# Kernel optimization log

Measured on AMD Instinct MI355X. Metric: run time of the kernel, lower is better.

## Reference

```python
import jax, jax.numpy as jnp
import numpy as np

KERNEL_SIZE = 4  # kernel_size=4, dim=1, degree-1 open B-splines (SplineConv defaults)


def spline_conv(x, edge_index, edge_attr, W, root, bias):
    """SplineConv with dim=1, kernel_size=4, degree=1, open splines, aggr='mean'.

    x: [N, F_in]; edge_index: [2, E] (row 0 = source, row 1 = target);
    edge_attr: [E, 1] pseudo-coords in [0,1]; W: [K, F_in, F_out];
    root: [F_in, F_out]; bias: [F_out].
    """
    N = x.shape[0]
    src, dst = edge_index[0], edge_index[1]
    u = edge_attr[:, 0]                          # [E]
    v = u * (KERNEL_SIZE - 1)                    # open spline: scale by K-1
    vf = jnp.floor(v)
    frac = v - vf                                # [E], degree-1 basis fraction
    k0 = jnp.clip(vf.astype(jnp.int32), 0, KERNEL_SIZE - 1)
    k1 = jnp.minimum(k0 + 1, KERNEL_SIZE - 1)
    # Project node features through all K kernel weights once: [N, K, F_out]
    xw = jnp.einsum('nf,kfo->nko', x, W)
    # Per-edge message: basis-weighted mix of the two active kernel projections
    m = (1.0 - frac)[:, None] * xw[src, k0] + frac[:, None] * xw[src, k1]  # [E, F_out]
    # Mean aggregation at target nodes
    agg = jax.ops.segment_sum(m, dst, num_segments=N)               # [N, F_out]
    deg = jax.ops.segment_sum(jnp.ones_like(u), dst, num_segments=N)
    agg = agg / jnp.maximum(deg, 1.0)[:, None]
    return agg + x @ root + bias


def setup_inputs() -> dict:
    key = jax.random.key(0)
    ks = jax.random.split(key, 9)
    N, E, F_IN, HID, C = 50000, 1600000, 48, 32, 10
    x = jax.random.normal(ks[0], (N, F_IN), dtype=jnp.float32)
    edge_index = jax.random.randint(ks[1], (2, E), 0, N, dtype=jnp.int64)
    edge_attr = jax.random.uniform(ks[2], (E, 1), dtype=jnp.float32)
    s = 0.1
    W1 = jax.random.normal(ks[3], (KERNEL_SIZE, F_IN, HID), dtype=jnp.float32) * s
    root1 = jax.random.normal(ks[4], (F_IN, HID), dtype=jnp.float32) * s
    bias1 = jax.random.normal(ks[5], (HID,), dtype=jnp.float32) * s
    W2 = jax.random.normal(ks[6], (KERNEL_SIZE, HID, C), dtype=jnp.float32) * s
    root2 = jax.random.normal(ks[7], (HID, C), dtype=jnp.float32) * s
    bias2 = jax.random.normal(ks[8], (C,), dtype=jnp.float32) * s
    return {"x": x, "edge_index": edge_index, "edge_attr": edge_attr,
            "W1": W1, "root1": root1, "bias1": bias1,
            "W2": W2, "root2": root2, "bias2": bias2}


def reference(x, edge_index, edge_attr, W1, root1, bias1, W2, root2, bias2):
    # dropout is identity in eval mode (training=self.training)
    h = spline_conv(x, edge_index, edge_attr, W1, root1, bias1)
    h = jax.nn.elu(h)
    h = spline_conv(h, edge_index, edge_attr, W2, root2, bias2)
    return jax.nn.log_softmax(h, axis=1)
```

## Files before the change

kernel.cpp:

```cpp
#include <hip/hip_runtime.h>
#include <math.h>


#define F_IN   48
#define HID    32
#define NCLS   10
#define KS     4
#define BKT_SH 8
#define TILE   4096

__device__ inline unsigned short f2bf(float f) {
    unsigned x = __float_as_uint(f);
    unsigned r = x + 0x7FFFu + ((x >> 16) & 1u);
    return (unsigned short)(r >> 16);
}
__device__ inline float bf2f(unsigned short u) {
    return __uint_as_float(((unsigned)u) << 16);
}


__global__ void bucket_hist_kernel(const int* __restrict__ ei, int* __restrict__ bcnt,
                                   int E, int NB) {
    __shared__ int lcnt[256];
    int t = threadIdx.x;
    lcnt[t] = 0;
    __syncthreads();
    int e0 = blockIdx.x * TILE;
    int n = min(TILE, E - e0);
    for (int r = 0; r < TILE / 256; ++r) {
        int i = r * 256 + t;
        if (i < n) atomicAdd(&lcnt[ei[E + e0 + i] >> BKT_SH], 1);
    }
    __syncthreads();
    if (t < NB && lcnt[t] > 0) atomicAdd(&bcnt[t], lcnt[t]);
}

__global__ void mini_scan_kernel(const int* __restrict__ bcnt, int* __restrict__ bbase,
                                 int* __restrict__ gcur, int NB) {
    __shared__ int a[256], c[256];
    int t = threadIdx.x;
    int v = (t < NB) ? bcnt[t] : 0;
    a[t] = v; c[t] = v;
    __syncthreads();
    for (int o = 1; o < 256; o <<= 1) {
        int w = (t >= o) ? a[t - o] : 0;
        __syncthreads();
        a[t] += w;
        __syncthreads();
    }
    int ex = a[t] - c[t];
    if (t < NB) { bbase[t] = ex; gcur[t] = ex; }
    if (t == 0) bbase[NB] = a[255];
}

__global__ void bucket_scatter_kernel(const int* __restrict__ ei, const float* __restrict__ ea,
                                      int* __restrict__ gcur, uint2* __restrict__ tpd,
                                      int E, int NB) {
    __shared__ unsigned spl[TILE];
    __shared__ unsigned short sdst[TILE];
    __shared__ unsigned short inv[TILE];
    __shared__ int lcnt[256], loff[256], lrank[256], gb[256];
    int t = threadIdx.x;
    lcnt[t] = 0; lrank[t] = 0;
    __syncthreads();
    int e0 = blockIdx.x * TILE;
    int n = min(TILE, E - e0);
    for (int r = 0; r < TILE / 256; ++r) {
        int i = r * 256 + t;
        if (i < n) {
            int e = e0 + i;
            int src = ei[e];
            int dst = ei[E + e];
            float u = ea[e];
            float v = u * (float)(KS - 1);
            float vf = floorf(v);
            int k0 = min(max((int)vf, 0), KS - 1);
            unsigned qf = (unsigned)((v - vf) * 16383.f + 0.5f);
            spl[i] = (unsigned)src | ((unsigned)k0 << 16) | (qf << 18);
            sdst[i] = (unsigned short)dst;
            atomicAdd(&lcnt[dst >> BKT_SH], 1);
        }
    }
    __syncthreads();
    loff[t] = lcnt[t];
    __syncthreads();
    for (int o = 1; o < 256; o <<= 1) {
        int w = (t >= o) ? loff[t - o] : 0;
        __syncthreads();
        loff[t] += w;
        __syncthreads();
    }
    int ex = loff[t] - lcnt[t];
    __syncthreads();
    loff[t] = ex;
    if (t < NB) gb[t] = atomicAdd(&gcur[t], lcnt[t]);
    __syncthreads();
    for (int r = 0; r < TILE / 256; ++r) {
        int i = r * 256 + t;
        if (i < n) {
            int b = sdst[i] >> BKT_SH;
            int p = loff[b] + atomicAdd(&lrank[b], 1);
            inv[p] = (unsigned short)i;
        }
    }
    __syncthreads();
    for (int r = 0; r < TILE / 256; ++r) {
        int j = r * 256 + t;
        if (j < n) {
            int i = inv[j];
            int d = sdst[i];
            int b = d >> BKT_SH;
            int pos = gb[b] + (j - loff[b]);
            tpd[pos] = make_uint2(spl[i], (unsigned)d);
        }
    }
}

__global__ void node_sort_kernel(const uint2* __restrict__ tpd, const int* __restrict__ bbase,
                                 unsigned* __restrict__ spk, int* __restrict__ offs,
                                 int N, int NB) {
    __shared__ int hc[256], hs[256], hr[256];
    int b = blockIdx.x;
    int t = threadIdx.x;
    int nb0 = b << BKT_SH;
    int nb = min(256, N - nb0);
    int base = bbase[b];
    int m = bbase[b + 1] - base;
    hc[t] = 0; hr[t] = 0;
    __syncthreads();
    for (int i = t; i < m; i += 256) atomicAdd(&hc[tpd[base + i].y - nb0], 1);
    __syncthreads();
    hs[t] = hc[t];
    __syncthreads();
    for (int o = 1; o < 256; o <<= 1) {
        int w = (t >= o) ? hs[t - o] : 0;
        __syncthreads();
        hs[t] += w;
        __syncthreads();
    }
    if (t < nb) offs[nb0 + t] = base + (hs[t] - hc[t]);
    if (b == NB - 1 && t == 0) offs[N] = base + m;
    for (int i = t; i < m; i += 256) {
        uint2 rec = tpd[base + i];
        int d = rec.y - nb0;
        int p = (hs[d] - hc[d]) + atomicAdd(&hr[d], 1);
        spk[base + p] = rec.x;
    }
}


__global__ __launch_bounds__(320) void xw1_kernel(
        const float* __restrict__ X, const float* __restrict__ W,
        const float* __restrict__ R, unsigned short* __restrict__ outk,
        float* __restrict__ outr, int n) {
    __shared__ float lw[48 * 160];
    int t = threadIdx.x;
    for (int i = t; i < 48 * 160; i += 320) {
        int f = i / 160;
        int col = i - f * 160;
        lw[i] = (col < 128) ? W[(size_t)(col >> 5) * (48 * 32) + f * 32 + (col & 31)]
                            : R[f * 32 + (col - 128)];
    }
    __syncthreads();
    int g = t % 40;
    int lp = t / 40;
    int n0 = (blockIdx.x * 8 + lp) * 2;
    if (n0 + 1 >= n) return;
    const float4* X0 = (const float4*)(X + (size_t)n0 * F_IN);
    const float4* X1 = (const float4*)(X + (size_t)(n0 + 1) * F_IN);
    float4 x0[12], x1[12];
#pragma unroll
    for (int i = 0; i < 12; ++i) { x0[i] = X0[i]; x1[i] = X1[i]; }
    const float4* lw4 = (const float4*)lw;
    float4 a0 = {0,0,0,0}, a1 = {0,0,0,0};
#pragma unroll
    for (int fb = 0; fb < 12; ++fb) {
        float4 v0 = x0[fb], v1 = x1[fb];
#pragma unroll
        for (int j = 0; j < 4; ++j) {
            float s0 = (j == 0) ? v0.x : (j == 1) ? v0.y : (j == 2) ? v0.z : v0.w;
            float s1 = (j == 0) ? v1.x : (j == 1) ? v1.y : (j == 2) ? v1.z : v1.w;
            float4 w = lw4[(fb * 4 + j) * 40 + g];
            a0.x = fmaf(s0, w.x, a0.x); a0.y = fmaf(s0, w.y, a0.y);
            a0.z = fmaf(s0, w.z, a0.z); a0.w = fmaf(s0, w.w, a0.w);
            a1.x = fmaf(s1, w.x, a1.x); a1.y = fmaf(s1, w.y, a1.y);
            a1.z = fmaf(s1, w.z, a1.z); a1.w = fmaf(s1, w.w, a1.w);
        }
    }
    if (g < 32) {
        uint2 u0, u1;
        u0.x = f2bf(a0.x) | ((unsigned)f2bf(a0.y) << 16);
        u0.y = f2bf(a0.z) | ((unsigned)f2bf(a0.w) << 16);
        u1.x = f2bf(a1.x) | ((unsigned)f2bf(a1.y) << 16);
        u1.y = f2bf(a1.z) | ((unsigned)f2bf(a1.w) << 16);
        *(uint2*)(outk + (size_t)n0 * (KS * HID) + g * 4) = u0;
        *(uint2*)(outk + (size_t)(n0 + 1) * (KS * HID) + g * 4) = u1;
    } else {
        int o = 4 * g - 128;
        *(float4*)(outr + (size_t)n0 * HID + o) = a0;
        *(float4*)(outr + (size_t)(n0 + 1) * HID + o) = a1;
    }
}

__global__ void xw2_kernel(const float* __restrict__ H, const float* __restrict__ W,
                           const float* __restrict__ R, unsigned short* __restrict__ outk,
                           float* __restrict__ outr, int n) {
    __shared__ float lw2[32 * 50];
    int t = threadIdx.x;
    for (int i = t; i < 32 * 50; i += 256) {
        int f = i / 50;
        int col = i - f * 50;
        lw2[i] = (col < 40) ? W[(size_t)(col / 10) * (32 * 10) + f * 10 + (col % 10)]
                            : R[f * 10 + (col - 40)];
    }
    __syncthreads();
    int total = (n / 2) * 25;
    int id = blockIdx.x * blockDim.x + t;
    if (id >= total) return;
    int p = id % 25;
    int pr = id / 25;
    int n0 = 2 * pr;
    const float4* H0 = (const float4*)(H + (size_t)n0 * HID);
    const float4* H1 = (const float4*)(H + (size_t)(n0 + 1) * HID);
    float4 h0[8], h1[8];
#pragma unroll
    for (int i = 0; i < 8; ++i) { h0[i] = H0[i]; h1[i] = H1[i]; }
    const float2* lwp = (const float2*)lw2;
    float ax0 = 0.f, ay0 = 0.f, ax1 = 0.f, ay1 = 0.f;
#pragma unroll
    for (int fb = 0; fb < 8; ++fb) {
        float4 v0 = h0[fb], v1 = h1[fb];
#pragma unroll
        for (int j = 0; j < 4; ++j) {
            float s0 = (j == 0) ? v0.x : (j == 1) ? v0.y : (j == 2) ? v0.z : v0.w;
            float s1 = (j == 0) ? v1.x : (j == 1) ? v1.y : (j == 2) ? v1.z : v1.w;
            float2 w = lwp[(fb * 4 + j) * 25 + p];
            ax0 = fmaf(s0, w.x, ax0); ay0 = fmaf(s0, w.y, ay0);
            ax1 = fmaf(s1, w.x, ax1); ay1 = fmaf(s1, w.y, ay1);
        }
    }
    int col = 2 * p;
    if (col < KS * NCLS) {
        *(unsigned*)(outk + (size_t)n0 * (KS * NCLS) + col) =
            f2bf(ax0) | ((unsigned)f2bf(ay0) << 16);
        *(unsigned*)(outk + (size_t)(n0 + 1) * (KS * NCLS) + col) =
            f2bf(ax1) | ((unsigned)f2bf(ay1) << 16);
    } else {
        int o = col - KS * NCLS;
        *(float2*)(outr + (size_t)n0 * NCLS + o) = make_float2(ax0, ay0);
        *(float2*)(outr + (size_t)(n0 + 1) * NCLS + o) = make_float2(ax1, ay1);
    }
}


__device__ inline float interp32(const unsigned short* __restrict__ xwk, unsigned p, int c) {
    int src = p & 0xFFFF;
    int k0 = (p >> 16) & 3;
    int k1 = min(k0 + 1, KS - 1);
    float fr = (float)(p >> 18) * (1.f / 16383.f);
    const unsigned short* row = xwk + (size_t)src * (KS * HID);
    float v0 = bf2f(row[k0 * HID + c]);
    float v1 = bf2f(row[k1 * HID + c]);
    return fmaf(fr, v1 - v0, v0);
}

__global__ void agg1_kernel(const unsigned short* __restrict__ xwk,
                            const float* __restrict__ xroot,
                            const int* __restrict__ offs, const unsigned* __restrict__ spk,
                            const float* __restrict__ bias, float* __restrict__ h, int n) {
    int lane = threadIdx.x & 63;
    int c = lane & 31;
    int half = lane >> 5;
    int node = blockIdx.x * 4 + (threadIdx.x >> 6);
    if (node >= n) return;
    int beg = offs[node];
    int end = offs[node + 1];
    float s0 = 0.f, s1 = 0.f;
    int e = beg + half;
    while (e + 2 < end) {
        unsigned p0 = spk[e];
        unsigned p1 = spk[e + 2];
        s0 += interp32(xwk, p0, c);
        s1 += interp32(xwk, p1, c);
        e += 4;
    }
    if (e < end) s0 += interp32(xwk, spk[e], c);
    float sum = s0 + s1;
    sum += __shfl_xor(sum, 32, 64);
    int deg = end - beg;
    float m = sum / (float)(deg > 0 ? deg : 1);
    float o = m + xroot[(size_t)node * HID + c] + bias[c];
    if (half == 0) h[(size_t)node * HID + c] = (o > 0.f) ? o : expm1f(o);
}

__device__ inline float interp10(const unsigned short* __restrict__ xwk, unsigned p, int cc) {
    int src = p & 0xFFFF;
    int k0 = (p >> 16) & 3;
    int k1 = min(k0 + 1, KS - 1);
    float fr = (float)(p >> 18) * (1.f / 16383.f);
    const unsigned short* row = xwk + (size_t)src * (KS * NCLS);
    float v0 = bf2f(row[k0 * NCLS + cc]);
    float v1 = bf2f(row[k1 * NCLS + cc]);
    return fmaf(fr, v1 - v0, v0);
}

__global__ void agg2_kernel(const unsigned short* __restrict__ xwk,
                            const float* __restrict__ xroot,
                            const int* __restrict__ offs, const unsigned* __restrict__ spk,
                            const float* __restrict__ bias, float* __restrict__ out, int n) {
    int g = threadIdx.x & 31;
    int c = g & 15;
    int par = g >> 4;
    int node = blockIdx.x * 8 + (threadIdx.x >> 5);
    if (node >= n) return;
    int cc = min(c, NCLS - 1);
    int beg = offs[node];
    int end = offs[node + 1];
    float s0 = 0.f, s1 = 0.f;
    int e = beg + par;
    while (e + 2 < end) {
        unsigned p0 = spk[e];
        unsigned p1 = spk[e + 2];
        s0 += interp10(xwk, p0, cc);
        s1 += interp10(xwk, p1, cc);
        e += 4;
    }
    if (e < end) s0 += interp10(xwk, spk[e], cc);
    float sum = s0 + s1;
    sum += __shfl_xor(sum, 16, 32);
    int deg = end - beg;
    float m = sum / (float)(deg > 0 ? deg : 1);
    float logit = m + xroot[(size_t)node * NCLS + cc] + bias[cc];
    bool active = (c < NCLS);
    float mx = active ? logit : -INFINITY;
#pragma unroll
    for (int msk = 1; msk < 16; msk <<= 1) mx = fmaxf(mx, __shfl_xor(mx, msk, 16));
    float ex = active ? expf(logit - mx) : 0.f;
    float s = ex;
#pragma unroll
    for (int msk = 1; msk < 16; msk <<= 1) s += __shfl_xor(s, msk, 16);
    if (active && par == 0) out[(size_t)node * NCLS + c] = (logit - mx) - logf(s);
}

extern "C" void kernel_launch(void* const* d_in, const int* in_sizes, int n_in,
                              void* d_out, int out_size, void* d_ws, size_t ws_size,
                              hipStream_t stream) {
    const float* x       = (const float*)d_in[0];
    const int*   ei      = (const int*)d_in[1];
    const float* ea      = (const float*)d_in[2];
    const float* W1      = (const float*)d_in[3];
    const float* root1   = (const float*)d_in[4];
    const float* bias1   = (const float*)d_in[5];
    const float* W2      = (const float*)d_in[6];
    const float* root2   = (const float*)d_in[7];
    const float* bias2   = (const float*)d_in[8];
    float* out = (float*)d_out;

    const int N = in_sizes[0] / F_IN;
    const int E = in_sizes[2];
    const int NB = (N + 255) >> BKT_SH;

    char* base = (char*)d_ws;
    size_t off = 0;
    auto alloc = [&](size_t bytes) {
        char* p = base + off;
        off = (off + bytes + 255) & ~(size_t)255;
        return (void*)p;
    };
    unsigned short* xwk1 = (unsigned short*)alloc((size_t)N * KS * HID * 2);
    float* xr1           = (float*)alloc((size_t)N * HID * 4);
    float* h             = (float*)alloc((size_t)N * HID * 4);
    int* offs            = (int*)alloc(((size_t)N + 1) * 4);
    int* bcnt            = (int*)alloc((size_t)NB * 4);
    int* bbase           = (int*)alloc(((size_t)NB + 1) * 4);
    int* gcur            = (int*)alloc((size_t)NB * 4);
    unsigned* spk        = (unsigned*)alloc((size_t)E * 4);
    uint2* tpd           = (uint2*)xwk1;
    unsigned short* xwk2 = xwk1;
    float* xr2           = xr1;
    if (ws_size < off) return;

    int ebk = (E + TILE - 1) / TILE;

    hipMemsetAsync(bcnt, 0, (size_t)NB * 4, stream);
    bucket_hist_kernel<<<ebk, 256, 0, stream>>>(ei, bcnt, E, NB);
    mini_scan_kernel<<<1, 256, 0, stream>>>(bcnt, bbase, gcur, NB);
    bucket_scatter_kernel<<<ebk, 256, 0, stream>>>(ei, ea, gcur, tpd, E, NB);
    node_sort_kernel<<<NB, 256, 0, stream>>>(tpd, bbase, spk, offs, N, NB);
    xw1_kernel<<<(N + 15) / 16, 320, 0, stream>>>(x, W1, root1, xwk1, xr1, N);
    agg1_kernel<<<(N + 3) / 4, 256, 0, stream>>>(xwk1, xr1, offs, spk, bias1, h, N);
    {
        int total = (N / 2) * 25;
        xw2_kernel<<<(total + 255) / 256, 256, 0, stream>>>(h, W2, root2, xwk2, xr2, N);
    }
    agg2_kernel<<<(N + 7) / 8, 256, 0, stream>>>(xwk2, xr2, offs, spk, bias2, out, N);
}
```

Baseline: 269.6 us.

## Precompute packed adjacent-kernel bf16 pairs so each edge gathers one word

Edge packing now encodes src*3+k0 with the fraction taken relative to k0 clamped to 2. New pairify kernels build per-node tables holding the k and k+1 projections packed as one 32-bit bf16 pair, so the aggregation kernels do a single 4-byte gather per edge per channel instead of two 2-byte gathers. The layer-2 projection output is padded to a 16-wide stride. The aggregation loops are unrolled further with nontemporal loads of the edge stream, and agg2 now handles 4 edges in parallel per node. The cost is two extra pass kernels and a larger workspace with extra table traffic.

```diff
diff --git a/kernel.cpp b/kernel.cpp
--- a/kernel.cpp
+++ b/kernel.cpp
@@ -74,9 +74,10 @@
             float u = ea[e];
             float v = u * (float)(KS - 1);
             float vf = floorf(v);
-            int k0 = min(max((int)vf, 0), KS - 1);
-            unsigned qf = (unsigned)((v - vf) * 16383.f + 0.5f);
-            spl[i] = (unsigned)src | ((unsigned)k0 << 16) | (qf << 18);
+            int k0 = min(max((int)vf, 0), 2);
+            float fr = v - (float)k0;
+            unsigned qf = (unsigned)(fr * 16383.f + 0.5f);
+            spl[i] = (unsigned)(src * 3 + k0) | (qf << 18);
             sdst[i] = (unsigned short)dst;
             atomicAdd(&lcnt[dst >> BKT_SH], 1);
         }
@@ -240,32 +241,52 @@
         }
     }
     int col = 2 * p;
-    if (col < KS * NCLS) {
-        *(unsigned*)(outk + (size_t)n0 * (KS * NCLS) + col) =
+    if (col < 40) {
+        int k = col / 10;
+        int o = col - k * 10;
+        *(unsigned*)(outk + (size_t)n0 * 64 + k * 16 + o) =
             f2bf(ax0) | ((unsigned)f2bf(ay0) << 16);
-        *(unsigned*)(outk + (size_t)(n0 + 1) * (KS * NCLS) + col) =
+        *(unsigned*)(outk + (size_t)(n0 + 1) * 64 + k * 16 + o) =
             f2bf(ax1) | ((unsigned)f2bf(ay1) << 16);
     } else {
-        int o = col - KS * NCLS;
+        int o = col - 40;
         *(float2*)(outr + (size_t)n0 * NCLS + o) = make_float2(ax0, ay0);
         *(float2*)(outr + (size_t)(n0 + 1) * NCLS + o) = make_float2(ax1, ay1);
     }
 }
 
 
-__device__ inline float interp32(const unsigned short* __restrict__ xwk, unsigned p, int c) {
-    int src = p & 0xFFFF;
-    int k0 = (p >> 16) & 3;
-    int k1 = min(k0 + 1, KS - 1);
-    float fr = (float)(p >> 18) * (1.f / 16383.f);
-    const unsigned short* row = xwk + (size_t)src * (KS * HID);
-    float v0 = bf2f(row[k0 * HID + c]);
-    float v1 = bf2f(row[k1 * HID + c]);
-    return fmaf(fr, v1 - v0, v0);
-}
-
-__global__ void agg1_kernel(const unsigned short* __restrict__ xwk,
-                            const float* __restrict__ xroot,
+__global__ void pairify1_kernel(const unsigned short* __restrict__ in,
+                                unsigned* __restrict__ out, int total) {
+    int id = blockIdx.x * 256 + threadIdx.x;
+    if (id >= total) return;
+    int c = id & 31;
+    int rest = id >> 5;
+    int node = rest / 3;
+    int ib = (rest + node) * 32 + c;
+    out[id] = (unsigned)in[ib] | ((unsigned)in[ib + 32] << 16);
+}
+
+__global__ void pairify2_kernel(const unsigned short* __restrict__ in,
+                                unsigned* __restrict__ out, int total) {
+    int id = blockIdx.x * 256 + threadIdx.x;
+    if (id >= total) return;
+    int c = id & 15;
+    int rest = id >> 4;
+    int node = rest / 3;
+    int ib = (rest + node) * 16 + c;
+    out[id] = (unsigned)in[ib] | ((unsigned)in[ib + 16] << 16);
+}
+
+
+__device__ inline float ginterp(const unsigned* __restrict__ t, unsigned p, int rowlen) {
+    unsigned w = t[(p & 0x3FFFFu) * rowlen];
+    float v0 = bf2f((unsigned short)w);
+    float v1 = bf2f((unsigned short)(w >> 16));
+    return fmaf((float)(p >> 18) * (1.f / 16383.f), v1 - v0, v0);
+}
+
+__global__ void agg1_kernel(const unsigned* __restrict__ tbl, const float* __restrict__ xr,
                             const int* __restrict__ offs, const unsigned* __restrict__ spk,
                             const float* __restrict__ bias, float* __restrict__ h, int n) {
     int lane = threadIdx.x & 63;
@@ -273,64 +294,58 @@
     int half = lane >> 5;
     int node = blockIdx.x * 4 + (threadIdx.x >> 6);
     if (node >= n) return;
-    int beg = offs[node];
-    int end = offs[node + 1];
+    int beg = offs[node], end = offs[node + 1];
+    const unsigned* t = tbl + c;
+    float s0 = 0.f, s1 = 0.f, s2 = 0.f, s3 = 0.f;
+    int e = beg + half;
+    for (; e + 6 < end; e += 8) {
+        unsigned p0 = __builtin_nontemporal_load(spk + e);
+        unsigned p1 = __builtin_nontemporal_load(spk + e + 2);
+        unsigned p2 = __builtin_nontemporal_load(spk + e + 4);
+        unsigned p3 = __builtin_nontemporal_load(spk + e + 6);
+        s0 += ginterp(t, p0, 32);
+        s1 += ginterp(t, p1, 32);
+        s2 += ginterp(t, p2, 32);
+        s3 += ginterp(t, p3, 32);
+    }
+    for (; e < end; e += 2)
+        s0 += ginterp(t, __builtin_nontemporal_load(spk + e), 32);
+    float sum = (s0 + s1) + (s2 + s3);
+    sum += __shfl_xor(sum, 32, 64);
+    if (half == 0) {
+        int deg = end - beg;
+        float m = sum / (float)(deg > 0 ? deg : 1);
+        float o = m + xr[(size_t)node * HID + c] + bias[c];
+        h[(size_t)node * HID + c] = (o > 0.f) ? o : expm1f(o);
+    }
+}
+
+__global__ void agg2_kernel(const unsigned* __restrict__ tbl, const float* __restrict__ xr,
+                            const int* __restrict__ offs, const unsigned* __restrict__ spk,
+                            const float* __restrict__ bias, float* __restrict__ out, int n) {
+    int lane = threadIdx.x & 63;
+    int c = lane & 15;
+    int slot = lane >> 4;
+    int node = blockIdx.x * 4 + (threadIdx.x >> 6);
+    if (node >= n) return;
+    int beg = offs[node], end = offs[node + 1];
+    const unsigned* t = tbl + c;
     float s0 = 0.f, s1 = 0.f;
-    int e = beg + half;
-    while (e + 2 < end) {
-        unsigned p0 = spk[e];
-        unsigned p1 = spk[e + 2];
-        s0 += interp32(xwk, p0, c);
-        s1 += interp32(xwk, p1, c);
-        e += 4;
-    }
-    if (e < end) s0 += interp32(xwk, spk[e], c);
+    int e = beg + slot;
+    for (; e + 4 < end; e += 8) {
+        unsigned p0 = __builtin_nontemporal_load(spk + e);
+        unsigned p1 = __builtin_nontemporal_load(spk + e + 4);
+        s0 += ginterp(t, p0, 16);
+        s1 += ginterp(t, p1, 16);
+    }
+    if (e < end) s0 += ginterp(t, __builtin_nontemporal_load(spk + e), 16);
     float sum = s0 + s1;
+    sum += __shfl_xor(sum, 16, 64);
     sum += __shfl_xor(sum, 32, 64);
     int deg = end - beg;
     float m = sum / (float)(deg > 0 ? deg : 1);
-    float o = m + xroot[(size_t)node * HID + c] + bias[c];
-    if (half == 0) h[(size_t)node * HID + c] = (o > 0.f) ? o : expm1f(o);
-}
-
-__device__ inline float interp10(const unsigned short* __restrict__ xwk, unsigned p, int cc) {
-    int src = p & 0xFFFF;
-    int k0 = (p >> 16) & 3;
-    int k1 = min(k0 + 1, KS - 1);
-    float fr = (float)(p >> 18) * (1.f / 16383.f);
-    const unsigned short* row = xwk + (size_t)src * (KS * NCLS);
-    float v0 = bf2f(row[k0 * NCLS + cc]);
-    float v1 = bf2f(row[k1 * NCLS + cc]);
-    return fmaf(fr, v1 - v0, v0);
-}
-
-__global__ void agg2_kernel(const unsigned short* __restrict__ xwk,
-                            const float* __restrict__ xroot,
-                            const int* __restrict__ offs, const unsigned* __restrict__ spk,
-                            const float* __restrict__ bias, float* __restrict__ out, int n) {
-    int g = threadIdx.x & 31;
-    int c = g & 15;
-    int par = g >> 4;
-    int node = blockIdx.x * 8 + (threadIdx.x >> 5);
-    if (node >= n) return;
     int cc = min(c, NCLS - 1);
-    int beg = offs[node];
-    int end = offs[node + 1];
-    float s0 = 0.f, s1 = 0.f;
-    int e = beg + par;
-    while (e + 2 < end) {
-        unsigned p0 = spk[e];
-        unsigned p1 = spk[e + 2];
-        s0 += interp10(xwk, p0, cc);
-        s1 += interp10(xwk, p1, cc);
-        e += 4;
-    }
-    if (e < end) s0 += interp10(xwk, spk[e], cc);
-    float sum = s0 + s1;
-    sum += __shfl_xor(sum, 16, 32);
-    int deg = end - beg;
-    float m = sum / (float)(deg > 0 ? deg : 1);
-    float logit = m + xroot[(size_t)node * NCLS + cc] + bias[cc];
+    float logit = m + xr[(size_t)node * NCLS + cc] + bias[cc];
     bool active = (c < NCLS);
     float mx = active ? logit : -INFINITY;
 #pragma unroll
@@ -339,7 +354,7 @@
     float s = ex;
 #pragma unroll
     for (int msk = 1; msk < 16; msk <<= 1) s += __shfl_xor(s, msk, 16);
-    if (active && par == 0) out[(size_t)node * NCLS + c] = (logit - mx) - logf(s);
+    if (active && slot == 0) out[(size_t)node * NCLS + c] = (logit - mx) - logf(s);
 }
 
 extern "C" void kernel_launch(void* const* d_in, const int* in_sizes, int n_in,
@@ -367,17 +382,19 @@
         off = (off + bytes + 255) & ~(size_t)255;
         return (void*)p;
     };
-    unsigned short* xwk1 = (unsigned short*)alloc((size_t)N * KS * HID * 2);
-    float* xr1           = (float*)alloc((size_t)N * HID * 4);
-    float* h             = (float*)alloc((size_t)N * HID * 4);
-    int* offs            = (int*)alloc(((size_t)N + 1) * 4);
-    int* bcnt            = (int*)alloc((size_t)NB * 4);
-    int* bbase           = (int*)alloc(((size_t)NB + 1) * 4);
-    int* gcur            = (int*)alloc((size_t)NB * 4);
-    unsigned* spk        = (unsigned*)alloc((size_t)E * 4);
-    uint2* tpd           = (uint2*)xwk1;
-    unsigned short* xwk2 = xwk1;
-    float* xr2           = xr1;
+    unsigned short* xwk1p = (unsigned short*)alloc((size_t)N * 128 * 2);
+    unsigned* xwk1        = (unsigned*)alloc((size_t)N * 96 * 4);
+    float* xr1            = (float*)alloc((size_t)N * HID * 4);
+    float* h              = (float*)alloc((size_t)N * HID * 4);
+    float* xr2            = (float*)alloc((size_t)N * NCLS * 4);
+    int* offs             = (int*)alloc(((size_t)N + 1) * 4);
+    int* bcnt             = (int*)alloc((size_t)NB * 4);
+    int* bbase            = (int*)alloc(((size_t)NB + 1) * 4);
+    int* gcur             = (int*)alloc((size_t)NB * 4);
+    unsigned* spk         = (unsigned*)alloc((size_t)E * 4);
+    uint2* tpd            = (uint2*)xwk1p;
+    unsigned short* xwk2p = xwk1p;
+    unsigned* xwk2        = xwk1;
     if (ws_size < off) return;
 
     int ebk = (E + TILE - 1) / TILE;
@@ -387,11 +404,13 @@
     mini_scan_kernel<<<1, 256, 0, stream>>>(bcnt, bbase, gcur, NB);
     bucket_scatter_kernel<<<ebk, 256, 0, stream>>>(ei, ea, gcur, tpd, E, NB);
     node_sort_kernel<<<NB, 256, 0, stream>>>(tpd, bbase, spk, offs, N, NB);
-    xw1_kernel<<<(N + 15) / 16, 320, 0, stream>>>(x, W1, root1, xwk1, xr1, N);
+    xw1_kernel<<<(N + 15) / 16, 320, 0, stream>>>(x, W1, root1, xwk1p, xr1, N);
+    pairify1_kernel<<<(N * 96 + 255) / 256, 256, 0, stream>>>(xwk1p, xwk1, N * 96);
     agg1_kernel<<<(N + 3) / 4, 256, 0, stream>>>(xwk1, xr1, offs, spk, bias1, h, N);
     {
         int total = (N / 2) * 25;
-        xw2_kernel<<<(total + 255) / 256, 256, 0, stream>>>(h, W2, root2, xwk2, xr2, N);
-    }
-    agg2_kernel<<<(N + 7) / 8, 256, 0, stream>>>(xwk2, xr2, offs, spk, bias2, out, N);
-}
+        xw2_kernel<<<(total + 255) / 256, 256, 0, stream>>>(h, W2, root2, xwk2p, xr2, N);
+    }
+    pairify2_kernel<<<(N * 48 + 255) / 256, 256, 0, stream>>>(xwk2p, xwk2, N * 48);
+    agg2_kernel<<<(N + 3) / 4, 256, 0, stream>>>(xwk2, xr2, offs, spk, bias2, out, N);
+}
```

New measurement: 289.9 us. 1.08x slower.
